# Kernel optimization log

Measured on AMD Instinct MI355X. Metric: run time of the kernel, lower is better.

The kernel has to match this reference:

```python
import jax, jax.numpy as jnp
import numpy as np

B, IN, FS, S, H = 4096, 4096, 4096, 64, 512  # batch, input_size, first_size, shape_lstm, n_hidden
D = FS // S  # per-step feature for left/right (=64); up/down per-step feature = S (=64)


def _lstm_cell(x, h, c, Wih, Whh, bih, bhh):
    # standard torch LSTMCell gate order: i, f, g, o
    g = x @ Wih.T + bih + h @ Whh.T + bhh  # (B, 4H)
    i, f, gg, o = jnp.split(g, 4, axis=-1)
    c = jax.nn.sigmoid(f) * c + jax.nn.sigmoid(i) * jnp.tanh(gg)
    h = jax.nn.sigmoid(o) * jnp.tanh(c)
    return h, c


def setup_inputs() -> dict:
    key = jax.random.key(0)
    ks = jax.random.split(key, 20)
    def cell(k, d_in):
        k1, k2, k3, k4 = jax.random.split(k, 4)
        s = 1.0 / np.sqrt(H)
        return (jax.random.uniform(k1, (4 * H, d_in), jnp.float32, -s, s),
                jax.random.uniform(k2, (4 * H, H), jnp.float32, -s, s),
                jax.random.uniform(k3, (4 * H,), jnp.float32, -s, s),
                jax.random.uniform(k4, (4 * H,), jnp.float32, -s, s))
    Wih_l, Whh_l, bih_l, bhh_l = cell(ks[0], D)
    Wih_r, Whh_r, bih_r, bhh_r = cell(ks[1], D)
    Wih_d, Whh_d, bih_d, bhh_d = cell(ks[2], S)
    return {
        "x": jax.random.normal(ks[3], (B, IN), jnp.float32),
        "h0": jax.random.normal(ks[4], (4, B, H), jnp.float32),
        "c0": jax.random.normal(ks[5], (4, B, H), jnp.float32),
        "W1": jax.random.normal(ks[6], (FS, IN), jnp.float32) * (1.0 / np.sqrt(IN)),
        "b1": jnp.zeros((FS,), jnp.float32),
        "Wih_l": Wih_l, "Whh_l": Whh_l, "bih_l": bih_l, "bhh_l": bhh_l,
        "Wih_r": Wih_r, "Whh_r": Whh_r, "bih_r": bih_r, "bhh_r": bhh_r,
        "Wih_d": Wih_d, "Whh_d": Whh_d, "bih_d": bih_d, "bhh_d": bhh_d,
        "W3": jax.random.normal(ks[7], (10, 4 * H), jnp.float32) * (1.0 / np.sqrt(4 * H)),
        "b3": jnp.zeros((10,), jnp.float32),
    }


def reference(x, h0, c0, W1, b1, Wih_l, Whh_l, bih_l, bhh_l,
              Wih_r, Whh_r, bih_r, bhh_r, Wih_d, Whh_d, bih_d, bhh_d, W3, b3):
    feat = jax.nn.relu(x @ W1.T + b1)            # (B, FS); dropout=identity (eval)
    il = feat.reshape(B, S, D)
    x_left = jnp.transpose(il, (1, 0, 2))         # (S, B, D)
    x_right = x_left[::-1]
    x_up = jnp.transpose(il, (2, 0, 1))           # (D, B, S); loop uses first S steps
    x_down = x_up[::-1]

    def step(carry, xs):
        (hl, cl, hr, cr, hu, cu, hd, cd) = carry
        xl, xr, xu, xd = xs
        hl, cl = _lstm_cell(xl, hl, cl, Wih_l, Whh_l, bih_l, bhh_l)
        hr, cr = _lstm_cell(xr, hr, cr, Wih_r, Whh_r, bih_r, bhh_r)
        # original code uses the DOWN cell for both up and down directions
        hu, cu = _lstm_cell(xu, hu, cu, Wih_d, Whh_d, bih_d, bhh_d)
        hd, cd = _lstm_cell(xd, hd, cd, Wih_d, Whh_d, bih_d, bhh_d)
        return (hl, cl, hr, cr, hu, cu, hd, cd), None

    carry0 = (h0[0], c0[0], h0[1], c0[1], h0[2], c0[2], h0[3], c0[3])
    (hl, _, hr, _, hu, _, hd, _), _ = jax.lax.scan(
        step, carry0, (x_left[:S], x_right[:S], x_up[:S], x_down[:S]))
    out = jnp.concatenate([hl, hr, hu, hd], axis=1)  # (B, 4H)
    logits = out @ W3.T + b3
    return jax.nn.log_softmax(logits, axis=1)
```

## Files before the change

### kernel.cpp

```cpp
#include <hip/hip_runtime.h>
#include <cstddef>
#include <cstdint>

namespace {

constexpr int kB  = 4096;
constexpr int kIN = 4096;
constexpr int kFS = 4096;
constexpr int kS  = 64;
constexpr int kH  = 512;
constexpr int kNG = 2048;
constexpr int kKC = 576;

typedef __bf16 bf16_t;
typedef __bf16 bfrag  __attribute__((ext_vector_type(8)));
typedef __bf16 bf16v4 __attribute__((ext_vector_type(4)));
typedef float  f32x4  __attribute__((ext_vector_type(4)));

__device__ __forceinline__ void gload16(const void* g, void* l) {
  __builtin_amdgcn_global_load_lds(
      (const __attribute__((address_space(1))) void*)g,
      (__attribute__((address_space(3))) void*)l, 16, 0, 0);
}

__device__ __forceinline__ float sigf(float x) { return 1.0f / (1.0f + __expf(-x)); }
__device__ __forceinline__ float tanh_fast(float x) {
  float e = __expf(2.0f * x);
  return 1.0f - 2.0f / (e + 1.0f);
}

__device__ __forceinline__ f32x4 mfma16(bfrag a, bfrag b, f32x4 c) {
  return __builtin_amdgcn_mfma_f32_16x16x32_bf16(a, b, c, 0, 0, 0);
}


__global__ __launch_bounds__(256) void f2b4_kernel(const float* __restrict__ in,
                                                   bf16_t* __restrict__ out, int n4) {
  int i = blockIdx.x * 256 + threadIdx.x;
  if (i >= n4) return;
  float4 v = reinterpret_cast<const float4*>(in)[i];
  bf16v4 o = {(bf16_t)v.x, (bf16_t)v.y, (bf16_t)v.z, (bf16_t)v.w};
  *reinterpret_cast<bf16v4*>(out + (size_t)i * 4) = o;
}

__global__ __launch_bounds__(256) void pack_wcat2_kernel(
    const float* __restrict__ Wih_l, const float* __restrict__ Whh_l,
    const float* __restrict__ Wih_r, const float* __restrict__ Whh_r,
    const float* __restrict__ Wih_d, const float* __restrict__ Whh_d,
    bf16_t* __restrict__ wcat2) {
  const int total = 3 * 128 * 9 * 2 * 64 * 8;
  int idx = blockIdx.x * 256 + threadIdx.x;
  if (idx >= total) return;
  int e  = idx & 7;
  int l  = (idx >> 3) & 63;
  int kk = (idx >> 9) & 1;
  int r  = idx >> 10;
  int kt = r % 9;
  int matnb = r / 9;
  int mat = matnb >> 7;
  int nb  = matnb & 127;
  const int c = nb * 16 + (l & 15);
  const int g = (c >> 4) & 3;
  const int u = (c >> 6) * 16 + (c & 15);
  const int orow = g * kH + u;
  const int k = kt * 64 + kk * 32 + (l >> 4) * 8 + e;
  const float* Wih = (mat == 0) ? Wih_l : (mat == 1) ? Wih_r : Wih_d;
  const float* Whh = (mat == 0) ? Whh_l : (mat == 1) ? Whh_r : Whh_d;
  float v = (k < 64) ? Wih[(size_t)orow * 64 + k] : Whh[(size_t)orow * 512 + (k - 64)];
  wcat2[idx] = (bf16_t)v;
}

__global__ __launch_bounds__(256) void pack_bias_kernel(
    const float* __restrict__ bih_l, const float* __restrict__ bhh_l,
    const float* __restrict__ bih_r, const float* __restrict__ bhh_r,
    const float* __restrict__ bih_d, const float* __restrict__ bhh_d,
    float* __restrict__ biasc) {
  int idx = blockIdx.x * 256 + threadIdx.x;
  if (idx >= 3 * kNG) return;
  int mat = idx / kNG;
  int c = idx - mat * kNG;
  int g = (c >> 4) & 3;
  int u = (c >> 6) * 16 + (c & 15);
  int orow = g * kH + u;
  const float* bi = (mat == 0) ? bih_l : (mat == 1) ? bih_r : bih_d;
  const float* bh = (mat == 0) ? bhh_l : (mat == 1) ? bhh_r : bhh_d;
  biasc[idx] = bi[orow] + bh[orow];
}

__global__ __launch_bounds__(256) void pack_hc_kernel(const float* __restrict__ h0,
                                                      const float* __restrict__ c0,
                                                      bf16_t* __restrict__ hbuf0,
                                                      float* __restrict__ cbuf, int n) {
  int i = blockIdx.x * 256 + threadIdx.x;
  if (i >= n) return;
  hbuf0[i] = (bf16_t)h0[i];
  __builtin_nontemporal_store(c0[i], &cbuf[i]);
}

__global__ __launch_bounds__(256) void transpose64_kernel(const bf16_t* __restrict__ feat,
                                                          bf16_t* __restrict__ featT) {
  __shared__ bf16_t tile[64][65];
  const int b = blockIdx.x;
  const bf16_t* src = feat + (size_t)b * kFS;
  bf16_t* dst = featT + (size_t)b * kFS;
  for (int i = threadIdx.x; i < 4096; i += 256) tile[i >> 6][i & 63] = src[i];
  __syncthreads();
  for (int i = threadIdx.x; i < 4096; i += 256) dst[i] = tile[i & 63][i >> 6];
}


__global__ __launch_bounds__(256, 4) void gemm_feat_kernel(
    const bf16_t* __restrict__ X, const bf16_t* __restrict__ W,
    const float* __restrict__ b1, bf16_t* __restrict__ feat) {
  __shared__ bf16_t As[128 * 32];
  __shared__ bf16_t Bs[128 * 32];
  const int t = threadIdx.x;
  const int bid = blockIdx.x;
  const int widx = (bid & 7) * 128 + (bid >> 3);
  const int bm = widx & 31, bn = widx >> 5;
  const int w = t >> 6, l = t & 63;
  const int wm = (w >> 1) * 64, wn = (w & 1) * 64;
  const int sr = t >> 2;
  const int skS = ((t & 3) ^ ((t >> 3) & 3)) * 8;
  const int lr = l & 15;
  const int lkS = ((l >> 4) ^ ((l >> 1) & 3)) * 8;
  const int lrow4 = (l >> 4) * 4;

  f32x4 acc[4][4];
#pragma unroll
  for (int i = 0; i < 4; ++i)
#pragma unroll
    for (int j = 0; j < 4; ++j) acc[i][j] = (f32x4){0.f, 0.f, 0.f, 0.f};

  const bf16_t* ga = X + (size_t)(bm * 128 + sr) * kIN + skS;
  const bf16_t* gb = W + (size_t)(bn * 128 + sr) * kIN + skS;
  bf16_t* lA = As + w * 512;
  bf16_t* lB = Bs + w * 512;

  for (int kt = 0; kt < kIN / 32; ++kt) {
    gload16(ga, lA);
    gload16(ga + (size_t)64 * kIN, lA + 2048);
    gload16(gb, lB);
    gload16(gb + (size_t)64 * kIN, lB + 2048);
    ga += 32; gb += 32;
    __syncthreads();
    bfrag a[4], b[4];
#pragma unroll
    for (int mi = 0; mi < 4; ++mi)
      a[mi] = *reinterpret_cast<const bfrag*>(&As[(wm + mi * 16 + lr) * 32 + lkS]);
#pragma unroll
    for (int ni = 0; ni < 4; ++ni)
      b[ni] = *reinterpret_cast<const bfrag*>(&Bs[(wn + ni * 16 + lr) * 32 + lkS]);
#pragma unroll
    for (int mi = 0; mi < 4; ++mi)
#pragma unroll
      for (int ni = 0; ni < 4; ++ni)
        acc[mi][ni] = __builtin_amdgcn_mfma_f32_16x16x32_bf16(a[mi], b[ni], acc[mi][ni], 0, 0, 0);
    __syncthreads();
  }

#pragma unroll
  for (int ni = 0; ni < 4; ++ni) {
    const int col = bn * 128 + wn + ni * 16 + lr;
    const float bb = b1[col];
#pragma unroll
    for (int mi = 0; mi < 4; ++mi) {
#pragma unroll
      for (int r = 0; r < 4; ++r) {
        const int row = bm * 128 + wm + mi * 16 + lrow4 + r;
        float v = acc[mi][ni][r] + bb;
        feat[(size_t)row * kFS + col] = (bf16_t)fmaxf(v, 0.0f);
      }
    }
  }
}


__global__ __launch_bounds__(512, 1) void lstm_step_kernel(
    const bf16_t* __restrict__ feat, const bf16_t* __restrict__ featT,
    const bf16_t* __restrict__ wcat2, const float* __restrict__ biasc,
    const bf16_t* __restrict__ hin, bf16_t* __restrict__ hout,
    float* __restrict__ cbuf, int s) {
  extern __shared__ __align__(16) char smem[];

  const int t = threadIdx.x;
  const int l = t & 63, w = t >> 6;
  const int wr = w >> 2, wc = w & 3;
  const int lr = l & 15, lq = l >> 4;
  const int sx = lr & 7;
  const int srow = l >> 3;
  const int sslot = (l & 7) ^ (srow & 7);

  const int bid = blockIdx.x;
  const int widx = (bid & 7) * 64 + (bid >> 3);
  const int cell = widx >> 7;
  const int rwk = widx & 127;
  const int bm = rwk >> 3, bn = rwk & 7;

  const bf16_t* xsrc = (cell < 2) ? feat : featT;
  const int off = ((cell & 1) ? (63 - s) : s) * 64;
  const int mat = (cell < 2) ? cell : 2;
  const bf16_t* hc = hin + (size_t)cell * kB * kH;

  auto stageA = [&](int kt, int buf) {
    bf16_t* base = (bf16_t*)(smem + buf * 32768);
#pragma unroll
    for (int j = 0; j < 4; ++j) {
      const int row0 = j * 64 + w * 8;
      bf16_t* dst = base + row0 * 64;
      const bf16_t* src = (kt == 0)
          ? xsrc + (size_t)(bm * 256 + row0 + srow) * kFS + off + sslot * 8
          : hc + (size_t)(bm * 256 + row0 + srow) * kH + (kt - 1) * 64 + sslot * 8;
      gload16(src, dst);
    }
  };

  const size_t wb0 = ((size_t)mat * 128 + bn * 16 + wc * 4) * 9;
  auto loadB = [&](int kt, bfrag (&d)[8]) {
#pragma unroll
    for (int nn = 0; nn < 4; ++nn)
#pragma unroll
      for (int kk = 0; kk < 2; ++kk)
        d[nn * 2 + kk] = *reinterpret_cast<const bfrag*>(
            wcat2 + (((wb0 + (size_t)nn * 9 + kt) * 2 + kk) << 9) + l * 8);
  };

  f32x4 acc[8][4];
#pragma unroll
  for (int i = 0; i < 8; ++i)
#pragma unroll
    for (int j = 0; j < 4; ++j) acc[i][j] = (f32x4){0.f, 0.f, 0.f, 0.f};

  bfrag bA[8], bB[8];

  stageA(0, 0);
  loadB(0, bA);
  asm volatile("s_waitcnt vmcnt(0)" ::: "memory");
  __builtin_amdgcn_sched_barrier(0);
  __builtin_amdgcn_s_barrier();

#pragma unroll
  for (int kt = 0; kt < 9; ++kt) {
    const int cur = kt & 1;
    const bf16_t* As_ = (const bf16_t*)(smem + cur * 32768);
    bfrag (&bCur)[8] = (kt & 1) ? bB : bA;
    bfrag (&bNxt)[8] = (kt & 1) ? bA : bB;

    if (kt < 8) stageA(kt + 1, cur ^ 1);

    bfrag a[8];
#pragma unroll
    for (int mi = 0; mi < 4; ++mi)
#pragma unroll
      for (int kk = 0; kk < 2; ++kk)
        a[mi * 2 + kk] = *reinterpret_cast<const bfrag*>(
            As_ + (wr * 128 + mi * 16 + lr) * 64 + (((kk * 4 + lq) ^ sx) * 8));
    __builtin_amdgcn_s_setprio(1);
#pragma unroll
    for (int kk = 0; kk < 2; ++kk)
#pragma unroll
      for (int mi = 0; mi < 4; ++mi)
#pragma unroll
        for (int nn = 0; nn < 4; ++nn)
          acc[mi][nn] = mfma16(a[mi * 2 + kk], bCur[nn * 2 + kk], acc[mi][nn]);
    __builtin_amdgcn_s_setprio(0);

    if (kt < 8) loadB(kt + 1, bNxt);

#pragma unroll
    for (int mi = 0; mi < 4; ++mi)
#pragma unroll
      for (int kk = 0; kk < 2; ++kk)
        a[mi * 2 + kk] = *reinterpret_cast<const bfrag*>(
            As_ + (wr * 128 + 64 + mi * 16 + lr) * 64 + (((kk * 4 + lq) ^ sx) * 8));
    __builtin_amdgcn_s_setprio(1);
#pragma unroll
    for (int kk = 0; kk < 2; ++kk)
#pragma unroll
      for (int mi = 0; mi < 4; ++mi)
#pragma unroll
        for (int nn = 0; nn < 4; ++nn)
          acc[4 + mi][nn] = mfma16(a[mi * 2 + kk], bCur[nn * 2 + kk], acc[4 + mi][nn]);
    __builtin_amdgcn_s_setprio(0);
    __builtin_amdgcn_sched_barrier(0);

    if (kt < 8) {
      asm volatile("s_waitcnt vmcnt(8)" ::: "memory");
      __builtin_amdgcn_sched_barrier(0);
      __builtin_amdgcn_s_barrier();
    }
  }

  const float* biasn = biasc + mat * kNG + bn * 256 + wc * 64;
  const float bb0 = biasn[0 * 16 + lr];
  const float bb1 = biasn[1 * 16 + lr];
  const float bb2 = biasn[2 * 16 + lr];
  const float bb3 = biasn[3 * 16 + lr];
  const int u = (bn * 4 + wc) * 16 + lr;
  const int row0 = bm * 256 + wr * 128 + lq * 4;
#pragma unroll
  for (int mi = 0; mi < 8; ++mi) {
#pragma unroll
    for (int j = 0; j < 4; ++j) {
      const float iv = sigf(acc[mi][0][j] + bb0);
      const float fv = sigf(acc[mi][1][j] + bb1);
      const float gv = tanh_fast(acc[mi][2][j] + bb2);
      const float ov = sigf(acc[mi][3][j] + bb3);
      const int row = row0 + mi * 16 + j;
      const size_t cidx = ((size_t)cell * kB + row) * kH + u;
      const float cold = __builtin_nontemporal_load(&cbuf[cidx]);
      const float cn = fv * cold + iv * gv;
      __builtin_nontemporal_store(cn, &cbuf[cidx]);
      hout[cidx] = (bf16_t)(ov * tanh_fast(cn));
    }
  }
}


__global__ __launch_bounds__(256) void head_kernel(const bf16_t* __restrict__ hfin,
                                                   const float* __restrict__ W3,
                                                   const float* __restrict__ b3,
                                                   float* __restrict__ out) {
  const int b = blockIdx.x, t = threadIdx.x;
  const int l = t & 63, w = t >> 6;
  float acc[10];
#pragma unroll
  for (int j = 0; j < 10; ++j) acc[j] = 0.f;
  for (int k = t; k < 2048; k += 256) {
    const int cell = k >> 9, u = k & 511;
    const float hv = (float)hfin[((size_t)cell * kB + b) * kH + u];
#pragma unroll
    for (int j = 0; j < 10; ++j) acc[j] += hv * W3[j * 2048 + k];
  }
#pragma unroll
  for (int j = 0; j < 10; ++j)
#pragma unroll
    for (int o = 32; o > 0; o >>= 1) acc[j] += __shfl_down(acc[j], o, 64);
  __shared__ float wred[4][10];
  if (l == 0)
#pragma unroll
    for (int j = 0; j < 10; ++j) wred[w][j] = acc[j];
  __syncthreads();
  if (t == 0) {
    float logits[10];
#pragma unroll
    for (int j = 0; j < 10; ++j)
      logits[j] = wred[0][j] + wred[1][j] + wred[2][j] + wred[3][j] + b3[j];
    float mx = logits[0];
#pragma unroll
    for (int j = 1; j < 10; ++j) mx = fmaxf(mx, logits[j]);
    float se = 0.f;
#pragma unroll
    for (int j = 0; j < 10; ++j) se += expf(logits[j] - mx);
    const float lse = mx + logf(se);
#pragma unroll
    for (int j = 0; j < 10; ++j) out[(size_t)b * 10 + j] = logits[j] - lse;
  }
}

}

extern "C" void kernel_launch(void* const* d_in, const int* in_sizes, int n_in,
                              void* d_out, int out_size, void* d_ws, size_t ws_size,
                              hipStream_t stream) {
  const float* x     = (const float*)d_in[0];
  const float* h0    = (const float*)d_in[1];
  const float* c0    = (const float*)d_in[2];
  const float* W1    = (const float*)d_in[3];
  const float* b1    = (const float*)d_in[4];
  const float* Wih_l = (const float*)d_in[5];
  const float* Whh_l = (const float*)d_in[6];
  const float* bih_l = (const float*)d_in[7];
  const float* bhh_l = (const float*)d_in[8];
  const float* Wih_r = (const float*)d_in[9];
  const float* Whh_r = (const float*)d_in[10];
  const float* bih_r = (const float*)d_in[11];
  const float* bhh_r = (const float*)d_in[12];
  const float* Wih_d = (const float*)d_in[13];
  const float* Whh_d = (const float*)d_in[14];
  const float* bih_d = (const float*)d_in[15];
  const float* bhh_d = (const float*)d_in[16];
  const float* W3    = (const float*)d_in[17];
  const float* b3    = (const float*)d_in[18];
  float* out = (float*)d_out;

  char* p = (char*)d_ws;
  auto take = [&](size_t bytes) {
    char* r = p;
    p += (bytes + 255) & ~(size_t)255;
    return r;
  };
  bf16_t* xb    = (bf16_t*)take((size_t)kB * kIN * 2);
  bf16_t* w1b   = (bf16_t*)take((size_t)kFS * kIN * 2);
  bf16_t* feat  = (bf16_t*)take((size_t)kB * kFS * 2);
  bf16_t* wcat2 = (bf16_t*)take((size_t)3 * 128 * 9 * 2 * 64 * 8 * 2);
  float*  biasc = (float*)take((size_t)3 * kNG * 4);
  float*  cbuf  = (float*)take((size_t)4 * kB * kH * 4);
  bf16_t* featT = xb;
  bf16_t* hbuf  = w1b;
  const size_t HSZ = (size_t)4 * kB * kH;

  (void)hipFuncSetAttribute(reinterpret_cast<const void*>(&lstm_step_kernel),
                            hipFuncAttributeMaxDynamicSharedMemorySize, 65536);

  f2b4_kernel<<<(kB * kIN / 4) / 256, 256, 0, stream>>>(x, xb, kB * kIN / 4);
  f2b4_kernel<<<(kFS * kIN / 4) / 256, 256, 0, stream>>>(W1, w1b, kFS * kIN / 4);
  gemm_feat_kernel<<<dim3(1024), 256, 0, stream>>>(xb, w1b, b1, feat);
  transpose64_kernel<<<kB, 256, 0, stream>>>(feat, featT);
  {
    const int total = 3 * 128 * 9 * 2 * 64 * 8;
    pack_wcat2_kernel<<<(total + 255) / 256, 256, 0, stream>>>(
        Wih_l, Whh_l, Wih_r, Whh_r, Wih_d, Whh_d, wcat2);
  }
  pack_bias_kernel<<<(3 * kNG + 255) / 256, 256, 0, stream>>>(
      bih_l, bhh_l, bih_r, bhh_r, bih_d, bhh_d, biasc);
  pack_hc_kernel<<<(int)(HSZ / 256), 256, 0, stream>>>(h0, c0, hbuf, cbuf, (int)HSZ);

  for (int s = 0; s < 64; ++s) {
    lstm_step_kernel<<<dim3(512), 512, 65536, stream>>>(
        feat, featT, wcat2, biasc,
        hbuf + (size_t)(s & 1) * HSZ, hbuf + (size_t)((s + 1) & 1) * HSZ, cbuf, s);
  }
  head_kernel<<<kB, 256, 0, stream>>>(hbuf, W3, b3, out);
}
```

Measured before the change: 3.952 ms.

## Store LSTM cell state in bf16 and stage c/h through LDS for coalesced I/O

The cell-state buffer changes from fp32 to bf16, halving its memory traffic each step. The old cell state is prefetched into shared memory with async global-to-LDS loads during the last K iteration. The epilogue writes new c and h into LDS, then stores them to global memory as coalesced 16-byte vectors instead of scattered 2- and 4-byte accesses. Keeping the cell state in bf16 loses precision, and that error builds up over 64 recurrent steps.

After: 4.266 ms. 7.9% more time.

```diff
diff --git a/kernel.cpp b/kernel.cpp
--- a/kernel.cpp
+++ b/kernel.cpp
@@ -90,11 +90,11 @@
 __global__ __launch_bounds__(256) void pack_hc_kernel(const float* __restrict__ h0,
                                                       const float* __restrict__ c0,
                                                       bf16_t* __restrict__ hbuf0,
-                                                      float* __restrict__ cbuf, int n) {
+                                                      bf16_t* __restrict__ cbuf, int n) {
   int i = blockIdx.x * 256 + threadIdx.x;
   if (i >= n) return;
   hbuf0[i] = (bf16_t)h0[i];
-  __builtin_nontemporal_store(c0[i], &cbuf[i]);
+  cbuf[i]  = (bf16_t)c0[i];
 }
 
 __global__ __launch_bounds__(256) void transpose64_kernel(const bf16_t* __restrict__ feat,
@@ -180,7 +180,7 @@
     const bf16_t* __restrict__ feat, const bf16_t* __restrict__ featT,
     const bf16_t* __restrict__ wcat2, const float* __restrict__ biasc,
     const bf16_t* __restrict__ hin, bf16_t* __restrict__ hout,
-    float* __restrict__ cbuf, int s) {
+    bf16_t* __restrict__ cbuf, int s) {
   extern __shared__ __align__(16) char smem[];
 
   const int t = threadIdx.x;
@@ -201,6 +201,7 @@
   const int off = ((cell & 1) ? (63 - s) : s) * 64;
   const int mat = (cell < 2) ? cell : 2;
   const bf16_t* hc = hin + (size_t)cell * kB * kH;
+  bf16_t* cc = cbuf + (size_t)cell * kB * kH;
 
   auto stageA = [&](int kt, int buf) {
     bf16_t* base = (bf16_t*)(smem + buf * 32768);
@@ -215,6 +216,16 @@
     }
   };
 
+  auto stageC = [&]() {
+#pragma unroll
+    for (int q = 0; q < 4; ++q) {
+      const int rowg = (w * 4 + q) * 8 + (l >> 3);
+      bf16_t* dst = (bf16_t*)(smem + 32768) + (w * 4 + q) * 512;
+      const bf16_t* src = cc + (size_t)(bm * 256 + rowg) * kH + bn * 64 + (l & 7) * 8;
+      gload16(src, dst);
+    }
+  };
+
   const size_t wb0 = ((size_t)mat * 128 + bn * 16 + wc * 4) * 9;
   auto loadB = [&](int kt, bfrag (&d)[8]) {
 #pragma unroll
@@ -247,6 +258,7 @@
     bfrag (&bNxt)[8] = (kt & 1) ? bA : bB;
 
     if (kt < 8) stageA(kt + 1, cur ^ 1);
+    if (kt == 8) stageC();
 
     bfrag a[8];
 #pragma unroll
@@ -291,28 +303,47 @@
     }
   }
 
+  asm volatile("s_waitcnt vmcnt(0) lgkmcnt(0)" ::: "memory");
+  __builtin_amdgcn_sched_barrier(0);
+  __builtin_amdgcn_s_barrier();
+
+  char* cl = smem + 32768;
+  char* hl = smem;
   const float* biasn = biasc + mat * kNG + bn * 256 + wc * 64;
   const float bb0 = biasn[0 * 16 + lr];
   const float bb1 = biasn[1 * 16 + lr];
   const float bb2 = biasn[2 * 16 + lr];
   const float bb3 = biasn[3 * 16 + lr];
-  const int u = (bn * 4 + wc) * 16 + lr;
-  const int row0 = bm * 256 + wr * 128 + lq * 4;
+  const int ucol2 = (wc * 16 + lr) * 2;
 #pragma unroll
   for (int mi = 0; mi < 8; ++mi) {
 #pragma unroll
     for (int j = 0; j < 4; ++j) {
+      const int row = wr * 128 + mi * 16 + lq * 4 + j;
+      const int boff = row * 128 + ucol2;
+      const float cold = (float)*reinterpret_cast<const bf16_t*>(cl + boff);
       const float iv = sigf(acc[mi][0][j] + bb0);
       const float fv = sigf(acc[mi][1][j] + bb1);
       const float gv = tanh_fast(acc[mi][2][j] + bb2);
       const float ov = sigf(acc[mi][3][j] + bb3);
-      const int row = row0 + mi * 16 + j;
-      const size_t cidx = ((size_t)cell * kB + row) * kH + u;
-      const float cold = __builtin_nontemporal_load(&cbuf[cidx]);
       const float cn = fv * cold + iv * gv;
-      __builtin_nontemporal_store(cn, &cbuf[cidx]);
-      hout[cidx] = (bf16_t)(ov * tanh_fast(cn));
+      *reinterpret_cast<bf16_t*>(cl + boff) = (bf16_t)cn;
+      *reinterpret_cast<bf16_t*>(hl + boff) = (bf16_t)(ov * tanh_fast(cn));
     }
+  }
+  __syncthreads();
+
+  bf16_t* hdst = hout + (size_t)cell * kB * kH;
+  const size_t gbase = (size_t)(bm * 256) * kH + bn * 64;
+#pragma unroll
+  for (int q = 0; q < 4; ++q) {
+    const int i2 = q * 512 + t;
+    const int row = i2 >> 3, ch = i2 & 7;
+    const size_t ge = gbase + (size_t)row * kH + ch * 8;
+    const bfrag cv = *reinterpret_cast<const bfrag*>(cl + row * 128 + ch * 16);
+    const bfrag hv = *reinterpret_cast<const bfrag*>(hl + row * 128 + ch * 16);
+    __builtin_nontemporal_store(cv, reinterpret_cast<bfrag*>(cc + ge));
+    *reinterpret_cast<bfrag*>(hdst + ge) = hv;
   }
 }
 
@@ -395,7 +426,7 @@
   bf16_t* feat  = (bf16_t*)take((size_t)kB * kFS * 2);
   bf16_t* wcat2 = (bf16_t*)take((size_t)3 * 128 * 9 * 2 * 64 * 8 * 2);
   float*  biasc = (float*)take((size_t)3 * kNG * 4);
-  float*  cbuf  = (float*)take((size_t)4 * kB * kH * 4);
+  bf16_t* cbuf  = (bf16_t*)take((size_t)4 * kB * kH * 2);
   bf16_t* featT = xb;
   bf16_t* hbuf  = w1b;
   const size_t HSZ = (size_t)4 * kB * kH;
```
